# Performance work log

Measured on AMD Instinct MI355X. Metric: run time of the kernel, lower is better.

## Reference

```python
import jax, jax.numpy as jnp
import numpy as np
import math

ROPE_BASE = 10000.0

def rope(x):
    # rotate-half RoPE over the full feature dim. x: [B, S, D]
    B, S, D = x.shape
    half = D // 2
    inv_freq = 1.0 / (ROPE_BASE ** (jnp.arange(half, dtype=jnp.float32) / half))
    ang = jnp.arange(S, dtype=jnp.float32)[:, None] * inv_freq[None, :]  # [S, half]
    cos, sin = jnp.cos(ang), jnp.sin(ang)
    x1, x2 = x[..., :half], x[..., half:]
    return jnp.concatenate([x1 * cos - x2 * sin, x1 * sin + x2 * cos], axis=-1)

def setup_inputs() -> dict:
    key = jax.random.key(0)
    ks = jax.random.split(key, 10)
    B, S, D = 4, 2048, 2048
    scale = 1.0 / math.sqrt(D)
    x = jax.random.normal(ks[0], (B, S, D), dtype=jnp.float32)
    mask = jnp.broadcast_to(jnp.tril(jnp.ones((S, S), dtype=jnp.int32)), (B, S, S))
    Wq = jax.random.normal(ks[1], (D, D), dtype=jnp.float32) * scale
    bq = jax.random.normal(ks[2], (D,), dtype=jnp.float32) * 0.02
    Wk = jax.random.normal(ks[3], (D, D), dtype=jnp.float32) * scale
    bk = jax.random.normal(ks[4], (D,), dtype=jnp.float32) * 0.02
    Wv = jax.random.normal(ks[5], (D, D), dtype=jnp.float32) * scale
    bv = jax.random.normal(ks[6], (D,), dtype=jnp.float32) * 0.02
    Wo = jax.random.normal(ks[7], (D, D), dtype=jnp.float32) * scale
    bo = jax.random.normal(ks[8], (D,), dtype=jnp.float32) * 0.02
    return {"x": x, "mask": mask, "Wq": Wq, "bq": bq, "Wk": Wk, "bk": bk,
            "Wv": Wv, "bv": bv, "Wo": Wo, "bo": bo}

def reference(x, mask, Wq, bq, Wk, bk, Wv, bv, Wo, bo):
    # x: [B, S, D]; torch.nn.Linear convention: y = x @ W.T + b
    D = x.shape[-1]
    std = jnp.sqrt(jnp.asarray(D, dtype=x.dtype))
    q = jnp.einsum('bsd,ed->bse', x, Wq) + bq
    k = jnp.einsum('bsd,ed->bse', x, Wk) + bk
    v = jnp.einsum('bsd,ed->bse', x, Wv) + bv
    # cache=None prefill path: q sliced to last x.size(-2) positions (full seq here)
    Sq = x.shape[-2]
    q = rope(q)[:, -Sq:, :]
    k = rope(k)
    scores = jnp.einsum('bqd,bkd->bqk', q, k) / std  # [B, Sq, Sk]
    scores = jnp.where(mask[:, -Sq:, :] == 0, -jnp.inf, scores)
    attn = jax.nn.softmax(scores, axis=-1)  # dropout=0 (eval)
    ctx = jnp.einsum('bqk,bkd->bqd', attn, v)
    out = jnp.einsum('bqd,ed->bqe', ctx, Wo) + bo
    return out
```

## Files before the change

### kernel.cpp

```cpp
#include <hip/hip_runtime.h>
#include <stdint.h>
#include <math.h>

#define BLK 256

typedef __bf16 bf16x8 __attribute__((ext_vector_type(8)));
typedef float  f32x4  __attribute__((ext_vector_type(4)));

__device__ __forceinline__ uint16_t f2bf(float f) {
  uint32_t u = __float_as_uint(f);
  u += 0x7fffu + ((u >> 16) & 1u);
  return (uint16_t)(u >> 16);
}
__device__ __forceinline__ float bf2f(uint16_t h) {
  return __uint_as_float(((uint32_t)h) << 16);
}

__device__ __forceinline__ void load_lds16(const void* g, void* l) {
  __builtin_amdgcn_global_load_lds(
      (const __attribute__((address_space(1))) uint32_t*)g,
      (__attribute__((address_space(3))) uint32_t*)l,
      16, 0, 0);
}

__global__ __launch_bounds__(BLK)
void convert_all(const float* __restrict__ x, const float* __restrict__ wq,
                 const float* __restrict__ wk, const float* __restrict__ wv,
                 const float* __restrict__ wo,
                 uint16_t* __restrict__ xb, uint16_t* __restrict__ wqkv,
                 float* __restrict__ sums) {
  const long tid0 = (long)blockIdx.x * BLK + threadIdx.x;
  if (tid0 < 8192) sums[tid0] = 0.f;
  const long XG = 4194304;
  const long T  = XG + 4 * 1048576;
  for (long i = tid0; i < T; i += (long)gridDim.x * BLK) {
    const float* src; uint16_t* dst; long off, doff;
    if (i < XG) { src = x; dst = xb; off = i; doff = i; }
    else {
      const long j = i - XG;
      const int seg = (int)(j >> 20);
      off = j & 1048575;
      src = (seg == 0) ? wq : (seg == 1) ? wk : (seg == 2) ? wv : wo;
      dst = wqkv + ((long)seg << 22);
      if (seg < 2) {
        const int f = (int)(off >> 9);
        const int g = (int)(off & 511);
        const int c = (f < 1024) ? (f << 1) : (((f - 1024) << 1) | 1);
        doff = (long)c * 512 + g;
      } else doff = off;
    }
    float4 v = ((const float4*)src)[off];
    ushort4 o;
    o.x = f2bf(v.x); o.y = f2bf(v.y); o.z = f2bf(v.z); o.w = f2bf(v.w);
    ((ushort4*)dst)[doff] = o;
  }
}

template<int MODE, int MINW>
__global__ __launch_bounds__(BLK, MINW)
void gemm_bt(const uint16_t* __restrict__ A, int lda,
             const uint16_t* __restrict__ Bt, int ldb,
             const float* __restrict__ b0, const float* __restrict__ b1,
             const float* __restrict__ b2,
             void* __restrict__ Cv, int ldc,
             int K, long sAb, long sBb, long sCb,
             float scale, float* __restrict__ rowsum,
             uint16_t* __restrict__ Vt)
{
  int tile_m, tile_n, bz;
  if (MODE == 2) {
    const int t = blockIdx.x;
    int r = (int)((sqrtf(8.f * (float)t + 1.f) - 1.f) * 0.5f);
    while ((r + 1) * (r + 2) / 2 <= t) ++r;
    while (r * (r + 1) / 2 > t) --r;
    tile_m = r * 128;
    tile_n = (t - r * (r + 1) / 2) * 128;
    bz = blockIdx.z;
  } else if (MODE == 3) {
    bz = blockIdx.y & 3;
    tile_m = ((int)(gridDim.y >> 2) - 1 - (int)(blockIdx.y >> 2)) * 128;
    tile_n = blockIdx.x * 128;
  } else {
    tile_m = blockIdx.y * 128;
    tile_n = blockIdx.x * 128;
    bz = blockIdx.z;
  }
  A  += (long)bz * sAb;
  Bt += (long)bz * sBb;

  __shared__ __align__(16) uint16_t smem[16384];
  uint16_t* sA = smem;
  uint16_t* sB = smem + 8192;

  const int tid  = threadIdx.x;
  const int lane = tid & 63;
  const int wave = tid >> 6;
  const int quad = lane >> 4;
  const int l16  = lane & 15;
  const int x8   = l16 & 7;
  const int wm = (wave & 1) * 64;
  const int wn = (wave >> 1) * 64;

  f32x4 acc[4][4];
#pragma unroll
  for (int i = 0; i < 4; ++i)
#pragma unroll
    for (int j = 0; j < 4; ++j) acc[i][j] = (f32x4){0.f, 0.f, 0.f, 0.f};

  const uint16_t* gA[4]; const uint16_t* gB[4];
  uint16_t* lA[4]; uint16_t* lB[4];
#pragma unroll
  for (int i = 0; i < 4; ++i) {
    const int id = wave * 256 + i * 64 + lane;
    const int row = id >> 3;
    const int c = (id & 7) ^ (row & 7);
    gA[i] = A  + (long)(tile_m + row) * lda + c * 8;
    gB[i] = Bt + (long)(tile_n + row) * ldb + c * 8;
    lA[i] = sA + (wave * 256 + i * 64) * 8;
    lB[i] = sB + (wave * 256 + i * 64) * 8;
  }

  const int kend = (MODE == 3) ? min(K, tile_m + 128) : K;

  for (int kk = 0; kk < kend; kk += 64) {
#pragma unroll
    for (int i = 0; i < 4; ++i) {
      load_lds16(gA[i] + kk, lA[i]);
      load_lds16(gB[i] + kk, lB[i]);
    }
    __syncthreads();

#pragma unroll
    for (int s2 = 0; s2 < 2; ++s2) {
      const int slot = ((quad + s2 * 4) ^ x8) * 8;
      bf16x8 af[4], bfr[4];
#pragma unroll
      for (int mi = 0; mi < 4; ++mi)
        af[mi] = *(const bf16x8*)(sA + (wm + mi * 16 + l16) * 64 + slot);
#pragma unroll
      for (int ni = 0; ni < 4; ++ni)
        bfr[ni] = *(const bf16x8*)(sB + (wn + ni * 16 + l16) * 64 + slot);
#pragma unroll
      for (int mi = 0; mi < 4; ++mi)
#pragma unroll
        for (int ni = 0; ni < 4; ++ni)
          acc[mi][ni] = __builtin_amdgcn_mfma_f32_16x16x32_bf16(af[mi], bfr[ni], acc[mi][ni], 0, 0, 0);
    }
    __syncthreads();
  }

  const int crow0 = tile_m + wm + quad * 4;
  const int ccol0 = tile_n + wn + l16;

  if constexpr (MODE == 2) {
    const bool diag = (tile_m == tile_n);
    uint16_t* Pp = (uint16_t*)Cv + (long)bz * sCb;
    float* rs = rowsum + (long)bz * 2048;
#pragma unroll
    for (int mi = 0; mi < 4; ++mi) {
#pragma unroll
      for (int r = 0; r < 4; ++r) {
        const int row = crow0 + mi * 16 + r;
        float partial = 0.f;
#pragma unroll
        for (int ni = 0; ni < 4; ++ni) {
          const int col = ccol0 + ni * 16;
          const float e = (!diag || col <= row) ? __expf(acc[mi][ni][r] * scale) : 0.f;
          const uint16_t h = f2bf(e);
          partial += bf2f(h);
          Pp[(long)row * ldc + col] = h;
        }
#pragma unroll
        for (int o = 1; o < 16; o <<= 1) partial += __shfl_xor(partial, o, 64);
        if (l16 == 0) atomicAdd(rs + row, partial);
      }
    }
  } else if constexpr (MODE == 3) {
    uint16_t* Cp = (uint16_t*)Cv + (long)bz * sCb;
    const float* rs = rowsum + (long)bz * 2048;
#pragma unroll
    for (int mi = 0; mi < 4; ++mi) {
#pragma unroll
      for (int r = 0; r < 4; ++r) {
        const int row = crow0 + mi * 16 + r;
        const float inv = 1.f / rs[row];
#pragma unroll
        for (int ni = 0; ni < 4; ++ni)
          Cp[(long)row * ldc + ccol0 + ni * 16] = f2bf(acc[mi][ni][r] * inv);
      }
    }
  } else if constexpr (MODE == 1) {
    const int seg = tile_n >> 11;
    if (seg < 2) {
      const float* bp = seg ? b1 : b0;
      uint16_t* Cp = (uint16_t*)Cv;
#pragma unroll
      for (int ni = 0; ni < 4; ++ni) {
        const int col = ccol0 + ni * 16;
        const int cc = col & 2047;
        const float bb = bp[(cc >> 1) + (cc & 1) * 1024];
        const float invf = exp2f((float)(cc >> 1) * (-13.287712379549449f / 1024.f));
        const float sgn = (cc & 1) ? 1.f : -1.f;
#pragma unroll
        for (int mi = 0; mi < 4; ++mi) {
#pragma unroll
          for (int r = 0; r < 4; ++r) {
            const int row = crow0 + mi * 16 + r;
            const float v = acc[mi][ni][r] + bb;
            float sn, cs;
            __sincosf((float)(row & 2047) * invf, &sn, &cs);
            const float p = __shfl_xor(v, 1, 64);
            Cp[(long)row * 4096 + col] = f2bf(v * cs + p * sgn * sn);
          }
        }
      }
    } else {
#pragma unroll
      for (int ni = 0; ni < 4; ++ni) {
        const int cl = wn + l16 + ni * 16;
        const float bb = b2[(ccol0 + ni * 16) & 2047];
#pragma unroll
        for (int mi = 0; mi < 4; ++mi) {
          const int rl0 = wm + quad * 4 + mi * 16;
          union { uint16_t u16[4]; uint64_t u64; } pk;
#pragma unroll
          for (int r = 0; r < 4; ++r) pk.u16[r] = f2bf(acc[mi][ni][r] + bb);
          *(uint64_t*)(smem + cl * 128 + (rl0 ^ ((cl & 15) << 3))) = pk.u64;
        }
      }
      __syncthreads();
      const int fl = quad;
      const int t0 = l16 * 8;
      const int bno = tile_m >> 11;
      const int tokbase = tile_m & 2047;
      uint16_t* Vp = Vt + (long)bno * 4194304 + tokbase;
      const int featbase = tile_n - 4096;
#pragma unroll
      for (int jj = 0; jj < 8; ++jj) {
        const int c = jj * 16 + wave * 4 + fl;
        const uint16_t* srcp = smem + c * 128 + (t0 ^ ((c & 15) << 3));
        ulonglong2 v = *(const ulonglong2*)srcp;
        *(ulonglong2*)(Vp + (long)(featbase + c) * 2048 + t0) = v;
      }
    }
  } else {
#pragma unroll
    for (int ni = 0; ni < 4; ++ni) {
      const int col = ccol0 + ni * 16;
      const float bb = b0[col];
#pragma unroll
      for (int mi = 0; mi < 4; ++mi) {
#pragma unroll
        for (int r = 0; r < 4; ++r) {
          const long row = crow0 + mi * 16 + r;
          ((float*)Cv)[row * (long)ldc + col] = acc[mi][ni][r] * scale + bb;
        }
      }
    }
  }
}

extern "C" void kernel_launch(void* const* d_in, const int* in_sizes, int n_in,
                              void* d_out, int out_size, void* d_ws, size_t ws_size,
                              hipStream_t stream) {
  const long S = 2048, D = 2048;
  const long MD = 4 * S * D;
  const long DD = D * D;

  const float* x  = (const float*)d_in[0];
  const float* Wq = (const float*)d_in[2];
  const float* bq = (const float*)d_in[3];
  const float* Wk = (const float*)d_in[4];
  const float* bk = (const float*)d_in[5];
  const float* Wv = (const float*)d_in[6];
  const float* bv = (const float*)d_in[7];
  const float* Wo = (const float*)d_in[8];
  const float* bo = (const float*)d_in[9];

  uint16_t* Xb    = (uint16_t*)d_ws;
  uint16_t* Wqkvb = Xb + MD;
  uint16_t* QK    = Wqkvb + 4 * DD;
  uint16_t* Vt    = QK + 8192L * 4096;
  uint16_t* P     = Vt + MD;
  float*    sums  = (float*)(P + 4 * S * S);
  if (ws_size < 268435456ull) return;

  dim3 blk(BLK);

  convert_all<<<16384, blk, 0, stream>>>(x, Wq, Wk, Wv, Wo, Xb, Wqkvb, sums);

  gemm_bt<1, 3><<<dim3(48, 64, 1), blk, 0, stream>>>(
      Xb, 2048, Wqkvb, 2048, bq, bk, bv, QK, 4096,
      2048, 0, 0, 0, 1.f, nullptr, Vt);

  gemm_bt<2, 3><<<dim3(136, 1, 4), blk, 0, stream>>>(
      QK, 4096, QK + 2048, 4096, nullptr, nullptr, nullptr, P, 2048,
      2048, 2048L * 4096, 2048L * 4096, S * S,
      0.022097086912079608f, sums, nullptr);

  gemm_bt<3, 4><<<dim3(16, 64, 1), blk, 0, stream>>>(
      P, 2048, Vt, 2048, nullptr, nullptr, nullptr, Xb, 2048,
      2048, S * S, S * D, S * D, 1.f, sums, nullptr);

  gemm_bt<0, 4><<<dim3(16, 64, 1), blk, 0, stream>>>(
      Xb, 2048, Wqkvb + 3 * DD, 2048, bo, nullptr, nullptr, (float*)d_out, 2048,
      2048, 0, 0, 0, 1.f, nullptr, nullptr);
}
```

Before: 581.8 us.

## Add 256x256-tile pipelined GEMM kernel for QKV and output projections

Introduces a new 512-thread GEMM kernel with 256x256 output tiles, 128KB dynamic LDS double buffering, and split-phase prefetch interleaved with MFMA blocks using s_waitcnt, barriers and setprio. Workgroup ids are swizzled to group tiles for L2 locality. The QKV projection (with fused RoPE and V transpose) and the output projection now use this kernel, while the old 128-tile kernel stays for the attention GEMMs. Larger tiles cut global/LDS traffic per FLOP, but they lower occupancy and leave fewer workgroups (256 for the output projection), which can cause wave quantization on the CU count.

```diff
diff --git a/kernel.cpp b/kernel.cpp
--- a/kernel.cpp
+++ b/kernel.cpp
@@ -22,6 +22,8 @@
       (__attribute__((address_space(3))) uint32_t*)l,
       16, 0, 0);
 }
+
+#define MFMA16(a, b, c) __builtin_amdgcn_mfma_f32_16x16x32_bf16(a, b, c, 0, 0, 0)
 
 __global__ __launch_bounds__(BLK)
 void convert_all(const float* __restrict__ x, const float* __restrict__ wq,
@@ -53,6 +55,205 @@
     ushort4 o;
     o.x = f2bf(v.x); o.y = f2bf(v.y); o.z = f2bf(v.z); o.w = f2bf(v.w);
     ((ushort4*)dst)[doff] = o;
+  }
+}
+
+template<int MODE>
+__global__ __launch_bounds__(512, 2)
+void gemm256(const uint16_t* __restrict__ A, const uint16_t* __restrict__ Bt,
+             const float* __restrict__ b0, const float* __restrict__ b1,
+             const float* __restrict__ b2, void* __restrict__ Cv,
+             uint16_t* __restrict__ Vt)
+{
+  constexpr int LD = 2048;
+  constexpr int NT = 32;
+  extern __shared__ ulonglong2 smem_raw[];
+  uint16_t* smem = (uint16_t*)smem_raw;
+
+  const int tid  = threadIdx.x;
+  const int lane = tid & 63;
+  const int wave = tid >> 6;
+  const int quad = lane >> 4;
+  const int l16  = lane & 15;
+  const int rsw  = (l16 >> 1) & 3;
+
+  const int nx   = gridDim.x;
+  const int nwg  = nx * gridDim.y;
+  const int wgid = blockIdx.y * nx + blockIdx.x;
+  const int sw   = (wgid & 7) * (nwg >> 3) + (wgid >> 3);
+  const int tile_n = (sw % nx) << 8;
+  const int tile_m = (sw / nx) << 8;
+
+  const int wm = (wave & 1) << 7;
+  const int wn = (wave >> 1) << 6;
+
+  const int srow = tid >> 2;
+  const int wch  = (((tid & 3) ^ ((tid >> 3) & 3)) << 3);
+  const uint16_t* gA = A  + (long)(tile_m + srow) * LD + wch;
+  const uint16_t* gB = Bt + (long)(tile_n + srow) * LD + wch;
+
+  f32x4 acc[8][4];
+#pragma unroll
+  for (int i = 0; i < 8; ++i)
+#pragma unroll
+    for (int j = 0; j < 4; ++j) acc[i][j] = (f32x4){0.f, 0.f, 0.f, 0.f};
+
+  auto stage2 = [&](int bufoff, const uint16_t* g0, int moff, int s, int kk) {
+    const uint16_t* g = g0 + kk + s * 32;
+    uint16_t* l = smem + bufoff + moff + s * 8192 + (wave << 9);
+    load_lds16(g, l);
+    load_lds16(g + 128 * LD, l + 4096);
+  };
+
+  const int raoff = (wm + l16) * 32;
+  const int rboff = 16384 + (wn + l16) * 32;
+  const int psw   = (quad ^ rsw) << 3;
+
+  stage2(0, gA, 0, 0, 0); stage2(0, gB, 16384, 0, 0);
+  stage2(0, gA, 0, 1, 0); stage2(0, gB, 16384, 1, 0);
+  asm volatile("s_waitcnt vmcnt(0)" ::: "memory");
+  __builtin_amdgcn_s_barrier();
+  asm volatile("" ::: "memory");
+
+  for (int t = 0; t < NT; ++t) {
+    const int cur = (t & 1) << 15;
+    const int oth = 32768 - cur;
+    const int kk1 = (t + 1) << 6;
+    const bool pf = (t + 1 < NT);
+    const uint16_t* bc = smem + cur;
+    bf16x8 af[8], bq0, bq1;
+
+    if (pf) stage2(oth, gA, 0, 0, kk1);
+    if (pf) { asm volatile("s_waitcnt vmcnt(6)" ::: "memory"); }
+    else    { asm volatile("s_waitcnt vmcnt(4)" ::: "memory"); }
+    __builtin_amdgcn_s_barrier();
+    asm volatile("" ::: "memory");
+#pragma unroll
+    for (int mi = 0; mi < 8; ++mi)
+      af[mi] = *(const bf16x8*)(bc + raoff + mi * 512 + psw);
+    bq0 = *(const bf16x8*)(bc + rboff + 0 * 512 + psw);
+    bq1 = *(const bf16x8*)(bc + rboff + 1 * 512 + psw);
+    __builtin_amdgcn_s_setprio(1);
+#pragma unroll
+    for (int mi = 0; mi < 8; ++mi) {
+      acc[mi][0] = MFMA16(af[mi], bq0, acc[mi][0]);
+      acc[mi][1] = MFMA16(af[mi], bq1, acc[mi][1]);
+    }
+    __builtin_amdgcn_s_setprio(0);
+    __builtin_amdgcn_s_barrier();
+
+    if (pf) stage2(oth, gB, 16384, 0, kk1);
+    bq0 = *(const bf16x8*)(bc + rboff + 2 * 512 + psw);
+    bq1 = *(const bf16x8*)(bc + rboff + 3 * 512 + psw);
+    __builtin_amdgcn_s_setprio(1);
+#pragma unroll
+    for (int mi = 0; mi < 8; ++mi) {
+      acc[mi][2] = MFMA16(af[mi], bq0, acc[mi][2]);
+      acc[mi][3] = MFMA16(af[mi], bq1, acc[mi][3]);
+    }
+    __builtin_amdgcn_s_setprio(0);
+    __builtin_amdgcn_s_barrier();
+
+    if (pf) stage2(oth, gA, 0, 1, kk1);
+    if (pf) { asm volatile("s_waitcnt vmcnt(6)" ::: "memory"); }
+    else    { asm volatile("s_waitcnt vmcnt(0)" ::: "memory"); }
+    __builtin_amdgcn_s_barrier();
+    asm volatile("" ::: "memory");
+#pragma unroll
+    for (int mi = 0; mi < 8; ++mi)
+      af[mi] = *(const bf16x8*)(bc + 8192 + raoff + mi * 512 + psw);
+    bq0 = *(const bf16x8*)(bc + 8192 + rboff + 0 * 512 + psw);
+    bq1 = *(const bf16x8*)(bc + 8192 + rboff + 1 * 512 + psw);
+    __builtin_amdgcn_s_setprio(1);
+#pragma unroll
+    for (int mi = 0; mi < 8; ++mi) {
+      acc[mi][0] = MFMA16(af[mi], bq0, acc[mi][0]);
+      acc[mi][1] = MFMA16(af[mi], bq1, acc[mi][1]);
+    }
+    __builtin_amdgcn_s_setprio(0);
+    __builtin_amdgcn_s_barrier();
+
+    if (pf) stage2(oth, gB, 16384, 1, kk1);
+    bq0 = *(const bf16x8*)(bc + 8192 + rboff + 2 * 512 + psw);
+    bq1 = *(const bf16x8*)(bc + 8192 + rboff + 3 * 512 + psw);
+    __builtin_amdgcn_s_setprio(1);
+#pragma unroll
+    for (int mi = 0; mi < 8; ++mi) {
+      acc[mi][2] = MFMA16(af[mi], bq0, acc[mi][2]);
+      acc[mi][3] = MFMA16(af[mi], bq1, acc[mi][3]);
+    }
+    __builtin_amdgcn_s_setprio(0);
+    __builtin_amdgcn_s_barrier();
+  }
+
+  const int crow0 = tile_m + wm + (quad << 2);
+  const int ccol0 = tile_n + wn + l16;
+
+  if constexpr (MODE == 1) {
+    const int seg = tile_n >> 11;
+    if (seg < 2) {
+      const float* bp = seg ? b1 : b0;
+      uint16_t* Cp = (uint16_t*)Cv;
+#pragma unroll
+      for (int ni = 0; ni < 4; ++ni) {
+        const int col = ccol0 + ni * 16;
+        const int cc = col & 2047;
+        const float bb = bp[(cc >> 1) + (cc & 1) * 1024];
+        const float invf = exp2f((float)(cc >> 1) * (-13.287712379549449f / 1024.f));
+        const float sgn = (cc & 1) ? 1.f : -1.f;
+#pragma unroll
+        for (int mi = 0; mi < 8; ++mi) {
+#pragma unroll
+          for (int r = 0; r < 4; ++r) {
+            const int row = crow0 + mi * 16 + r;
+            const float v = acc[mi][ni][r] + bb;
+            float sn, cs;
+            __sincosf((float)(row & 2047) * invf, &sn, &cs);
+            const float p = __shfl_xor(v, 1, 64);
+            Cp[(long)row * 4096 + col] = f2bf(v * cs + p * sgn * sn);
+          }
+        }
+      }
+    } else {
+      uint16_t* ws = smem + wave * 8192;
+#pragma unroll
+      for (int ni = 0; ni < 4; ++ni) {
+        const int f = ni * 16 + l16;
+        const float bb = b2[(ccol0 + ni * 16) & 2047];
+#pragma unroll
+        for (int mi = 0; mi < 8; ++mi) {
+          const int t0 = mi * 16 + (quad << 2);
+          union { uint16_t u16[4]; uint64_t u64; } pk;
+#pragma unroll
+          for (int r = 0; r < 4; ++r) pk.u16[r] = f2bf(acc[mi][ni][r] + bb);
+          *(uint64_t*)(ws + f * 128 + (t0 ^ ((f & 15) << 3))) = pk.u64;
+        }
+      }
+      __syncthreads();
+      const int bno      = (tile_m + wm) >> 11;
+      const int tokbase  = (tile_m + wm) & 2047;
+      const int featbase = tile_n - 4096 + wn;
+      uint16_t* Vp = Vt + (long)bno * 4194304 + tokbase;
+#pragma unroll
+      for (int jj = 0; jj < 16; ++jj) {
+        const int f = jj * 4 + quad;
+        const uint16_t* srcp = ws + f * 128 + ((l16 * 8) ^ ((f & 15) << 3));
+        ulonglong2 v = *(const ulonglong2*)srcp;
+        *(ulonglong2*)(Vp + (long)(featbase + f) * 2048 + l16 * 8) = v;
+      }
+    }
+  } else {
+    float* Co = (float*)Cv;
+#pragma unroll
+    for (int ni = 0; ni < 4; ++ni) {
+      const int col = ccol0 + ni * 16;
+      const float bb = b0[col];
+#pragma unroll
+      for (int mi = 0; mi < 8; ++mi)
+#pragma unroll
+        for (int r = 0; r < 4; ++r)
+          Co[(long)(crow0 + mi * 16 + r) * 2048 + col] = acc[mi][ni][r] + bb;
+    }
   }
 }
 
@@ -144,7 +345,7 @@
       for (int mi = 0; mi < 4; ++mi)
 #pragma unroll
         for (int ni = 0; ni < 4; ++ni)
-          acc[mi][ni] = __builtin_amdgcn_mfma_f32_16x16x32_bf16(af[mi], bfr[ni], acc[mi][ni], 0, 0, 0);
+          acc[mi][ni] = MFMA16(af[mi], bfr[ni], acc[mi][ni]);
     }
     __syncthreads();
   }
@@ -187,74 +388,6 @@
 #pragma unroll
         for (int ni = 0; ni < 4; ++ni)
           Cp[(long)row * ldc + ccol0 + ni * 16] = f2bf(acc[mi][ni][r] * inv);
-      }
-    }
-  } else if constexpr (MODE == 1) {
-    const int seg = tile_n >> 11;
-    if (seg < 2) {
-      const float* bp = seg ? b1 : b0;
-      uint16_t* Cp = (uint16_t*)Cv;
-#pragma unroll
-      for (int ni = 0; ni < 4; ++ni) {
-        const int col = ccol0 + ni * 16;
-        const int cc = col & 2047;
-        const float bb = bp[(cc >> 1) + (cc & 1) * 1024];
-        const float invf = exp2f((float)(cc >> 1) * (-13.287712379549449f / 1024.f));
-        const float sgn = (cc & 1) ? 1.f : -1.f;
-#pragma unroll
-        for (int mi = 0; mi < 4; ++mi) {
-#pragma unroll
-          for (int r = 0; r < 4; ++r) {
-            const int row = crow0 + mi * 16 + r;
-            const float v = acc[mi][ni][r] + bb;
-            float sn, cs;
-            __sincosf((float)(row & 2047) * invf, &sn, &cs);
-            const float p = __shfl_xor(v, 1, 64);
-            Cp[(long)row * 4096 + col] = f2bf(v * cs + p * sgn * sn);
-          }
-        }
-      }
-    } else {
-#pragma unroll
-      for (int ni = 0; ni < 4; ++ni) {
-        const int cl = wn + l16 + ni * 16;
-        const float bb = b2[(ccol0 + ni * 16) & 2047];
-#pragma unroll
-        for (int mi = 0; mi < 4; ++mi) {
-          const int rl0 = wm + quad * 4 + mi * 16;
-          union { uint16_t u16[4]; uint64_t u64; } pk;
-#pragma unroll
-          for (int r = 0; r < 4; ++r) pk.u16[r] = f2bf(acc[mi][ni][r] + bb);
-          *(uint64_t*)(smem + cl * 128 + (rl0 ^ ((cl & 15) << 3))) = pk.u64;
-        }
-      }
-      __syncthreads();
-      const int fl = quad;
-      const int t0 = l16 * 8;
-      const int bno = tile_m >> 11;
-      const int tokbase = tile_m & 2047;
-      uint16_t* Vp = Vt + (long)bno * 4194304 + tokbase;
-      const int featbase = tile_n - 4096;
-#pragma unroll
-      for (int jj = 0; jj < 8; ++jj) {
-        const int c = jj * 16 + wave * 4 + fl;
-        const uint16_t* srcp = smem + c * 128 + (t0 ^ ((c & 15) << 3));
-        ulonglong2 v = *(const ulonglong2*)srcp;
-        *(ulonglong2*)(Vp + (long)(featbase + c) * 2048 + t0) = v;
-      }
-    }
-  } else {
-#pragma unroll
-    for (int ni = 0; ni < 4; ++ni) {
-      const int col = ccol0 + ni * 16;
-      const float bb = b0[col];
-#pragma unroll
-      for (int mi = 0; mi < 4; ++mi) {
-#pragma unroll
-        for (int r = 0; r < 4; ++r) {
-          const long row = crow0 + mi * 16 + r;
-          ((float*)Cv)[row * (long)ldc + col] = acc[mi][ni][r] * scale + bb;
-        }
       }
     }
   }
@@ -285,13 +418,21 @@
   float*    sums  = (float*)(P + 4 * S * S);
   if (ws_size < 268435456ull) return;
 
+  static int once = []() {
+    hipFuncSetAttribute(reinterpret_cast<const void*>(&gemm256<1>),
+                        hipFuncAttributeMaxDynamicSharedMemorySize, 131072);
+    hipFuncSetAttribute(reinterpret_cast<const void*>(&gemm256<0>),
+                        hipFuncAttributeMaxDynamicSharedMemorySize, 131072);
+    return 0;
+  }();
+  (void)once;
+
   dim3 blk(BLK);
 
   convert_all<<<16384, blk, 0, stream>>>(x, Wq, Wk, Wv, Wo, Xb, Wqkvb, sums);
 
-  gemm_bt<1, 3><<<dim3(48, 64, 1), blk, 0, stream>>>(
-      Xb, 2048, Wqkvb, 2048, bq, bk, bv, QK, 4096,
-      2048, 0, 0, 0, 1.f, nullptr, Vt);
+  gemm256<1><<<dim3(24, 32), dim3(512), 131072, stream>>>(
+      Xb, Wqkvb, bq, bk, bv, QK, Vt);
 
   gemm_bt<2, 3><<<dim3(136, 1, 4), blk, 0, stream>>>(
       QK, 4096, QK + 2048, 4096, nullptr, nullptr, nullptr, P, 2048,
@@ -302,7 +443,6 @@
       P, 2048, Vt, 2048, nullptr, nullptr, nullptr, Xb, 2048,
       2048, S * S, S * D, S * D, 1.f, sums, nullptr);
 
-  gemm_bt<0, 4><<<dim3(16, 64, 1), blk, 0, stream>>>(
-      Xb, 2048, Wqkvb + 3 * DD, 2048, bo, nullptr, nullptr, (float*)d_out, 2048,
-      2048, 0, 0, 0, 1.f, nullptr, nullptr);
-}
+  gemm256<0><<<dim3(8, 32), dim3(512), 131072, stream>>>(
+      Xb, Wqkvb + 3 * DD, bo, nullptr, nullptr, (float*)d_out, nullptr);
+}
```

Result: slower. 610.3 us (+4.9%).
